# Optimization experiments

Hardware: AMD Instinct MI355X
Metric: run time of the kernel (lower is better)

The kernel has to match this reference:

```python
import jax, jax.numpy as jnp
import numpy as np

NEG = -1e9  # mask value for non-edges (matches masked_fill(-inf) numerically-safely)
SLOPE = 0.2  # LeakyReLU negative slope in GraphAttentionLayer


def gat_layer(x, W, a_l, a_r, adj, n_heads):
    """One GraphAttentionLayer (eval mode, is_concat=True).
    e[i,j,h] = leakyrelu(a_l . g[i,h] + a_r . g[j,h])  (attn Linear split into halves)
    softmax over j masked by adj, then aggregate neighbors.
    """
    n = x.shape[0]
    g = (x @ W).reshape(n, n_heads, -1)          # [n, h, f]
    el = jnp.einsum('ihf,f->ih', g, a_l)          # score contribution of node i
    er = jnp.einsum('jhf,f->jh', g, a_r)          # score contribution of node j
    e = jax.nn.leaky_relu(el[:, None, :] + er[None, :, :], SLOPE)  # [n, n, h]
    e = jnp.where(adj[:, :, None] != 0, e, NEG)
    a = jax.nn.softmax(e, axis=1)                 # softmax over neighbors j
    out = jnp.einsum('ijh,jhf->ihf', a, g)        # weighted aggregation
    return out.reshape(n, -1)                     # concat heads


def setup_inputs() -> dict:
    key = jax.random.key(0)
    ks = jax.random.split(key, 8)
    N, IN, HID, OUT, H = 2048, 512, 256, 128, 8
    x = jax.random.normal(ks[0], (N, IN), dtype=jnp.float32)
    adj = jax.random.randint(ks[1], (N, N), 0, 2, dtype=jnp.int32)
    adj = adj.at[jnp.arange(N), jnp.arange(N)].set(1)  # self loops: no empty softmax rows
    s = 0.05
    W1 = jax.random.normal(ks[2], (IN, HID), dtype=jnp.float32) * s
    a1_l = jax.random.normal(ks[3], (HID // H,), dtype=jnp.float32) * s
    a1_r = jax.random.normal(ks[4], (HID // H,), dtype=jnp.float32) * s
    W2 = jax.random.normal(ks[5], (HID, OUT), dtype=jnp.float32) * s
    a2_l = jax.random.normal(ks[6], (OUT,), dtype=jnp.float32) * s
    a2_r = jax.random.normal(ks[7], (OUT,), dtype=jnp.float32) * s
    return {"x": x, "W1": W1, "a1_l": a1_l, "a1_r": a1_r,
            "W2": W2, "a2_l": a2_l, "a2_r": a2_r, "adj_mat": adj}


def reference(x, W1, a1_l, a1_r, W2, a2_l, a2_r, adj_mat):
    # eval mode: nn.Dropout is identity
    h = gat_layer(x, W1, a1_l, a1_r, adj_mat, n_heads=8)
    h = jax.nn.elu(h)
    out = gat_layer(h, W2, a2_l, a2_r, adj_mat, n_heads=1)
    return out
```

## Files before the change

kernel.cpp:

```cpp
#include <hip/hip_runtime.h>
#include <hip/hip_bf16.h>

#define NN 2048
typedef unsigned short u16;
typedef unsigned long long u64;
typedef __attribute__((ext_vector_type(8))) short short8;
typedef __attribute__((ext_vector_type(4))) float f32x4;

__device__ __forceinline__ unsigned bfb(float x) {
    unsigned u = __float_as_uint(x);
    return (u + 0x7FFFu + ((u >> 16) & 1u)) >> 16;
}
__device__ __forceinline__ unsigned pk2(float a, float b) {
    unsigned r;
    asm("v_cvt_pk_bf16_f32 %0, %1, %2" : "=v"(r) : "v"(a), "v"(b));
    return r;
}

__global__ __launch_bounds__(256) void prep(const float* __restrict__ x,
                                            const float* __restrict__ W1,
                                            const float* __restrict__ W2,
                                            const int* __restrict__ adj,
                                            u16* __restrict__ xb, u16* __restrict__ w1t,
                                            u16* __restrict__ w2t, u64* __restrict__ ab) {
    const int b = blockIdx.x;
    const int tid = threadIdx.x;
    if (b < 2048) {
#pragma unroll
        for (int k = 0; k < 8; ++k) {
            int t = (b * 8 + k) * 256 + tid;
            int W = t >> 6, lane = t & 63;
            int i = W >> 5, jw = W & 31;
            int a = adj[(size_t)i * NN + jw * 64 + lane];
            u64 mk = __ballot(a != 0);
            if (lane == 0) ab[(size_t)i * 32 + jw] = mk;
        }
    } else if (b < 2048 + 256) {
#pragma unroll
        for (int k = 0; k < 4; ++k) {
            int t = ((b - 2048) * 4 + k) * 256 + tid;
            float4 v = ((const float4*)x)[t];
            uint2 o;
            o.x = pk2(v.x, v.y);
            o.y = pk2(v.z, v.w);
            ((uint2*)xb)[t] = o;
        }
    } else if (b < 2048 + 256 + 128) {
#pragma unroll
        for (int k = 0; k < 4; ++k) {
            int u = ((b - 2304) * 4 + k) * 256 + tid;
            int c = u >> 9, kk = u & 511;
            w1t[u] = (u16)bfb(W1[(size_t)kk * 256 + c]);
        }
    } else {
#pragma unroll
        for (int k = 0; k < 4; ++k) {
            int u = ((b - 2432) * 4 + k) * 256 + tid;
            int c = u >> 8, kk = u & 255;
            w2t[u] = (u16)bfb(W2[(size_t)kk * 128 + c]);
        }
    }
}

__global__ __launch_bounds__(256) void gemm1(const u16* __restrict__ A,
                                             const u16* __restrict__ BT,
                                             const float* __restrict__ al,
                                             const float* __restrict__ ar,
                                             u16* __restrict__ GT,
                                             float* __restrict__ el,
                                             float* __restrict__ ert) {
    const int i0 = blockIdx.x * 16, cs = blockIdx.y;
    const int t = threadIdx.x, lane = t & 63, w = t >> 6;
    const int q = lane >> 4, n = lane & 15;
    const int ct = w & 1, kh = w >> 1;
    __shared__ float osh[2][16][16];
    __shared__ float pel[2][16], per_[2][16];

    const u16* ap = A + (size_t)(i0 + n) * 512 + kh * 256 + q * 8;
    const u16* bp = BT + (size_t)(cs * 32 + ct * 16 + n) * 512 + kh * 256 + q * 8;
    f32x4 acc = {0.f, 0.f, 0.f, 0.f};
#pragma unroll
    for (int ks = 0; ks < 8; ++ks) {
        short8 a = *(const short8*)(ap + ks * 32);
        short8 b = *(const short8*)(bp + ks * 32);
        acc = __builtin_amdgcn_mfma_f32_16x16x32_bf16(a, b, acc, 0, 0, 0);
    }
    if (kh == 1) {
#pragma unroll
        for (int r = 0; r < 4; ++r) osh[ct][q * 4 + r][n] = acc[r];
    }
    __syncthreads();
    if (kh == 0) {
#pragma unroll
        for (int r = 0; r < 4; ++r) acc[r] += osh[ct][q * 4 + r][n];
        uint2 g0;
        g0.x = pk2(acc[0], acc[1]);
        g0.y = pk2(acc[2], acc[3]);
        *(uint2*)&GT[(size_t)(cs * 32 + ct * 16 + n) * NN + i0 + q * 4] = g0;
        const float alv = al[ct * 16 + n], arv = ar[ct * 16 + n];
#pragma unroll
        for (int r = 0; r < 4; ++r) {
            float ve = acc[r] * alv, vr = acc[r] * arv;
#pragma unroll
            for (int off = 1; off <= 8; off <<= 1) {
                ve += __shfl_xor(ve, off);
                vr += __shfl_xor(vr, off);
            }
            if (n == 0) { pel[ct][q * 4 + r] = ve; per_[ct][q * 4 + r] = vr; }
        }
    }
    __syncthreads();
    if (t < 16) {
        el[(size_t)(i0 + t) * 8 + cs] = pel[0][t] + pel[1][t];
        ert[(size_t)cs * NN + i0 + t] = per_[0][t] + per_[1][t];
    }
}

__global__ __launch_bounds__(256) void gemm2(const u16* __restrict__ A,
                                             const u16* __restrict__ BT,
                                             const float* __restrict__ al,
                                             const float* __restrict__ ar,
                                             u16* __restrict__ GT,
                                             float* __restrict__ el2p,
                                             float* __restrict__ er2p) {
    const int i0 = blockIdx.x * 16, cs = blockIdx.y;
    const int t = threadIdx.x, lane = t & 63, w = t >> 6;
    const int q = lane >> 4, n = lane & 15;
    const int ct = w & 1, kh = w >> 1;
    __shared__ float osh[2][16][16];
    __shared__ float pel[2][16], per_[2][16];

    const u16* ap = A + (size_t)(i0 + n) * 256 + kh * 128 + q * 8;
    const u16* bp = BT + (size_t)(cs * 32 + ct * 16 + n) * 256 + kh * 128 + q * 8;
    f32x4 acc = {0.f, 0.f, 0.f, 0.f};
#pragma unroll
    for (int ks = 0; ks < 4; ++ks) {
        short8 a = *(const short8*)(ap + ks * 32);
        short8 b = *(const short8*)(bp + ks * 32);
        acc = __builtin_amdgcn_mfma_f32_16x16x32_bf16(a, b, acc, 0, 0, 0);
    }
    if (kh == 1) {
#pragma unroll
        for (int r = 0; r < 4; ++r) osh[ct][q * 4 + r][n] = acc[r];
    }
    __syncthreads();
    if (kh == 0) {
#pragma unroll
        for (int r = 0; r < 4; ++r) acc[r] += osh[ct][q * 4 + r][n];
        uint2 g0;
        g0.x = pk2(acc[0], acc[1]);
        g0.y = pk2(acc[2], acc[3]);
        *(uint2*)&GT[(size_t)(cs * 32 + ct * 16 + n) * NN + i0 + q * 4] = g0;
        const float alv = al[cs * 32 + ct * 16 + n], arv = ar[cs * 32 + ct * 16 + n];
#pragma unroll
        for (int r = 0; r < 4; ++r) {
            float ve = acc[r] * alv, vr = acc[r] * arv;
#pragma unroll
            for (int off = 1; off <= 8; off <<= 1) {
                ve += __shfl_xor(ve, off);
                vr += __shfl_xor(vr, off);
            }
            if (n == 0) { pel[ct][q * 4 + r] = ve; per_[ct][q * 4 + r] = vr; }
        }
    }
    __syncthreads();
    if (t < 16) {
        el2p[(size_t)cs * NN + i0 + t] = pel[0][t] + pel[1][t];
        er2p[(size_t)cs * NN + i0 + t] = per_[0][t] + per_[1][t];
    }
}

__global__ __launch_bounds__(512, 4) void attn1(const float* __restrict__ el,
                                                const float* __restrict__ ert,
                                                const unsigned* __restrict__ ab32,
                                                const u16* __restrict__ gbt,
                                                u16* __restrict__ hbb) {
    const int rt = blockIdx.x, sec = blockIdx.y;
    const int i0 = rt * 16, h0 = sec * 2;
    const int t = threadIdx.x, lane = t & 63, w = t >> 6;
    const int q = lane >> 4, n = lane & 15;
    const int m = t >> 5, jq = t & 31;
    const int hl = w >> 2, ch = (w >> 1) & 1, kf2 = w & 1;

    __shared__ u16 ersb[2][2048];
    __shared__ __align__(16) u16 pl[2][2][16][264];
    __shared__ unsigned absh[16][64];
    __shared__ float psum_sh[16][2];
    __shared__ float osh[2][2][16][16];
    __shared__ float wmax[2][8];
    __shared__ float mxsh[2];

    float4 v0 = *(const float4*)(ert + (size_t)h0 * NN + t * 4);
    float4 v1 = *(const float4*)(ert + (size_t)(h0 + 1) * NN + t * 4);
    uint2 c0, c1;
    c0.x = pk2(v0.x, v0.y); c0.y = pk2(v0.z, v0.w);
    c1.x = pk2(v1.x, v1.y); c1.y = pk2(v1.z, v1.w);
    *(uint2*)&ersb[0][t * 4] = c0;
    *(uint2*)&ersb[1][t * 4] = c1;
    float m0 = fmaxf(fmaxf(v0.x, v0.y), fmaxf(v0.z, v0.w));
    float m1 = fmaxf(fmaxf(v1.x, v1.y), fmaxf(v1.z, v1.w));
#pragma unroll
    for (int off = 32; off; off >>= 1) {
        m0 = fmaxf(m0, __shfl_xor(m0, off));
        m1 = fmaxf(m1, __shfl_xor(m1, off));
    }
    if (lane == 0) { wmax[0][w] = m0; wmax[1][w] = m1; }
    for (int c = t; c < 1024; c += 512)
        absh[c >> 6][c & 63] = ab32[(size_t)(i0 + (c >> 6)) * 64 + (c & 63)];
    __syncthreads();
    if (t < 2) {
        float mm = wmax[t][0];
#pragma unroll
        for (int ww = 1; ww < 8; ++ww) mm = fmaxf(mm, wmax[t][ww]);
        mxsh[t] = mm;
    }
    __syncthreads();

    float elv[2], mxv[2], ps[2];
#pragma unroll
    for (int h = 0; h < 2; ++h) {
        float e = el[(size_t)(i0 + m) * 8 + h0 + h];
        elv[h] = e;
        float mm = e + mxsh[h];
        mxv[h] = fmaxf(mm, 0.2f * mm);
        ps[h] = 0.f;
    }

    auto stage = [&](int tl, int nb) {
#pragma unroll
        for (int sub = 0; sub < 2; ++sub) {
            unsigned word = absh[m][tl * 8 + sub * 4 + (jq >> 3)];
            unsigned bits = (word >> ((jq & 7) * 4)) & 0xFu;
            const int jo = tl * 256 + sub * 128 + jq * 4;
            uint2 raw0 = *(const uint2*)&ersb[0][jo];
            uint2 raw1 = *(const uint2*)&ersb[1][jo];
#pragma unroll
            for (int h = 0; h < 2; ++h) {
                uint2 raw = h ? raw1 : raw0;
                float e0 = __uint_as_float(raw.x << 16);
                float e1 = __uint_as_float(raw.x & 0xFFFF0000u);
                float e2 = __uint_as_float(raw.y << 16);
                float e3 = __uint_as_float(raw.y & 0xFFFF0000u);
                float s0 = elv[h] + e0, s1 = elv[h] + e1, s2 = elv[h] + e2, s3 = elv[h] + e3;
                s0 = fmaxf(s0, 0.2f * s0) - mxv[h];
                s1 = fmaxf(s1, 0.2f * s1) - mxv[h];
                s2 = fmaxf(s2, 0.2f * s2) - mxv[h];
                s3 = fmaxf(s3, 0.2f * s3) - mxv[h];
                float p0 = (bits & 1u) ? __expf(s0) : 0.f;
                float p1 = (bits & 2u) ? __expf(s1) : 0.f;
                float p2 = (bits & 4u) ? __expf(s2) : 0.f;
                float p3 = (bits & 8u) ? __expf(s3) : 0.f;
                ps[h] += (p0 + p1) + (p2 + p3);
                uint2 pkv;
                pkv.x = pk2(p0, p1);
                pkv.y = pk2(p2, p3);
                *(uint2*)&pl[nb][h][m][sub * 128 + jq * 4] = pkv;
            }
        }
    };

    const int col = sec * 64 + hl * 32 + ch * 16 + n;
    const u16* gb = gbt + (size_t)col * NN + kf2 * 128 + q * 8;
    short8 bc0 = *(const short8*)gb;
    short8 bc1 = *(const short8*)(gb + 32);
    short8 bc2 = *(const short8*)(gb + 64);
    short8 bc3 = *(const short8*)(gb + 96);
    f32x4 acc = {0.f, 0.f, 0.f, 0.f};

    stage(0, 0);
    __syncthreads();

    for (int tile = 0; tile < 8; ++tile) {
        short8 bn0 = bc0, bn1 = bc1, bn2 = bc2, bn3 = bc3;
        if (tile < 7) {
            const u16* gq = gb + (tile + 1) * 256;
            bn0 = *(const short8*)gq;
            bn1 = *(const short8*)(gq + 32);
            bn2 = *(const short8*)(gq + 64);
            bn3 = *(const short8*)(gq + 96);
        }
        const u16* ap = &pl[tile & 1][hl][n][kf2 * 128 + q * 8];
        short8 a0 = *(const short8*)ap;
        short8 a1 = *(const short8*)(ap + 32);
        short8 a2 = *(const short8*)(ap + 64);
        short8 a3 = *(const short8*)(ap + 96);
        acc = __builtin_amdgcn_mfma_f32_16x16x32_bf16(a0, bc0, acc, 0, 0, 0);
        acc = __builtin_amdgcn_mfma_f32_16x16x32_bf16(a1, bc1, acc, 0, 0, 0);
        acc = __builtin_amdgcn_mfma_f32_16x16x32_bf16(a2, bc2, acc, 0, 0, 0);
        acc = __builtin_amdgcn_mfma_f32_16x16x32_bf16(a3, bc3, acc, 0, 0, 0);
        if (tile < 7) stage(tile + 1, (tile + 1) & 1);
        bc0 = bn0; bc1 = bn1; bc2 = bn2; bc3 = bn3;
        __syncthreads();
    }

#pragma unroll
    for (int h = 0; h < 2; ++h) {
        float v = ps[h];
#pragma unroll
        for (int off = 16; off; off >>= 1) v += __shfl_down(v, off, 32);
        if (jq == 0) psum_sh[m][h] = v;
    }
    if (kf2 == 1) {
#pragma unroll
        for (int r = 0; r < 4; ++r) osh[hl][ch][q * 4 + r][n] = acc[r];
    }
    __syncthreads();
    if (kf2 == 0) {
#pragma unroll
        for (int r = 0; r < 4; ++r) {
            int mr = q * 4 + r;
            float o = (acc[r] + osh[hl][ch][mr][n]) / psum_sh[mr][hl];
            o = o > 0.f ? o : (__expf(o) - 1.f);
            hbb[(size_t)(i0 + mr) * 256 + col] = (u16)bfb(o);
        }
    }
}

__global__ __launch_bounds__(512) void attn2(const float* __restrict__ el2p,
                                             const float* __restrict__ er2p,
                                             const unsigned* __restrict__ ab32,
                                             const u16* __restrict__ gbt,
                                             float* __restrict__ out) {
    const int rt = blockIdx.x, sec = blockIdx.y;
    const int i0 = rt * 16;
    const int t = threadIdx.x, lane = t & 63, w = t >> 6;
    const int q = lane >> 4, n = lane & 15;
    const int m = t >> 5, jq = t & 31;
    const int ct = w >> 1, kf2 = w & 1;

    __shared__ u16 ersb[2048];
    __shared__ __align__(16) u16 pl[2][16][264];
    __shared__ unsigned absh[16][64];
    __shared__ float psum_sh[16];
    __shared__ float osh[4][16][16];
    __shared__ float wmax[8];
    __shared__ float mxsh;

    float4 a0 = *(const float4*)(er2p + t * 4);
    float4 a1 = *(const float4*)(er2p + NN + t * 4);
    float4 a2 = *(const float4*)(er2p + 2 * NN + t * 4);
    float4 a3 = *(const float4*)(er2p + 3 * NN + t * 4);
    float4 v0;
    v0.x = ((a0.x + a1.x) + (a2.x + a3.x));
    v0.y = ((a0.y + a1.y) + (a2.y + a3.y));
    v0.z = ((a0.z + a1.z) + (a2.z + a3.z));
    v0.w = ((a0.w + a1.w) + (a2.w + a3.w));
    uint2 c0;
    c0.x = pk2(v0.x, v0.y); c0.y = pk2(v0.z, v0.w);
    *(uint2*)&ersb[t * 4] = c0;
    float m0 = fmaxf(fmaxf(v0.x, v0.y), fmaxf(v0.z, v0.w));
#pragma unroll
    for (int off = 32; off; off >>= 1) m0 = fmaxf(m0, __shfl_xor(m0, off));
    if (lane == 0) wmax[w] = m0;
    for (int c = t; c < 1024; c += 512)
        absh[c >> 6][c & 63] = ab32[(size_t)(i0 + (c >> 6)) * 64 + (c & 63)];
    __syncthreads();
    if (t == 0) {
        float mm = wmax[0];
#pragma unroll
        for (int ww = 1; ww < 8; ++ww) mm = fmaxf(mm, wmax[ww]);
        mxsh = mm;
    }
    __syncthreads();

    const float elv = el2p[i0 + m] + el2p[NN + i0 + m] + el2p[2 * NN + i0 + m] + el2p[3 * NN + i0 + m];
    float mm2 = elv + mxsh;
    const float mxv = fmaxf(mm2, 0.2f * mm2);
    float ps = 0.f;

    auto stage = [&](int tl, int nb) {
#pragma unroll
        for (int sub = 0; sub < 2; ++sub) {
            unsigned word = absh[m][tl * 8 + sub * 4 + (jq >> 3)];
            unsigned bits = (word >> ((jq & 7) * 4)) & 0xFu;
            const int jo = tl * 256 + sub * 128 + jq * 4;
            uint2 raw = *(const uint2*)&ersb[jo];
            float e0 = __uint_as_float(raw.x << 16);
            float e1 = __uint_as_float(raw.x & 0xFFFF0000u);
            float e2 = __uint_as_float(raw.y << 16);
            float e3 = __uint_as_float(raw.y & 0xFFFF0000u);
            float s0 = elv + e0, s1 = elv + e1, s2 = elv + e2, s3 = elv + e3;
            s0 = fmaxf(s0, 0.2f * s0) - mxv;
            s1 = fmaxf(s1, 0.2f * s1) - mxv;
            s2 = fmaxf(s2, 0.2f * s2) - mxv;
            s3 = fmaxf(s3, 0.2f * s3) - mxv;
            float p0 = (bits & 1u) ? __expf(s0) : 0.f;
            float p1 = (bits & 2u) ? __expf(s1) : 0.f;
            float p2 = (bits & 4u) ? __expf(s2) : 0.f;
            float p3 = (bits & 8u) ? __expf(s3) : 0.f;
            ps += (p0 + p1) + (p2 + p3);
            uint2 pkv;
            pkv.x = pk2(p0, p1);
            pkv.y = pk2(p2, p3);
            *(uint2*)&pl[nb][m][sub * 128 + jq * 4] = pkv;
        }
    };

    const int col = sec * 64 + ct * 16 + n;
    const u16* gb = gbt + (size_t)col * NN + kf2 * 128 + q * 8;
    short8 bc0 = *(const short8*)gb;
    short8 bc1 = *(const short8*)(gb + 32);
    short8 bc2 = *(const short8*)(gb + 64);
    short8 bc3 = *(const short8*)(gb + 96);
    f32x4 acc = {0.f, 0.f, 0.f, 0.f};

    stage(0, 0);
    __syncthreads();

    for (int tile = 0; tile < 8; ++tile) {
        short8 bn0 = bc0, bn1 = bc1, bn2 = bc2, bn3 = bc3;
        if (tile < 7) {
            const u16* gq = gb + (tile + 1) * 256;
            bn0 = *(const short8*)gq;
            bn1 = *(const short8*)(gq + 32);
            bn2 = *(const short8*)(gq + 64);
            bn3 = *(const short8*)(gq + 96);
        }
        const u16* ap = &pl[tile & 1][n][kf2 * 128 + q * 8];
        short8 a0v = *(const short8*)ap;
        short8 a1v = *(const short8*)(ap + 32);
        short8 a2v = *(const short8*)(ap + 64);
        short8 a3v = *(const short8*)(ap + 96);
        acc = __builtin_amdgcn_mfma_f32_16x16x32_bf16(a0v, bc0, acc, 0, 0, 0);
        acc = __builtin_amdgcn_mfma_f32_16x16x32_bf16(a1v, bc1, acc, 0, 0, 0);
        acc = __builtin_amdgcn_mfma_f32_16x16x32_bf16(a2v, bc2, acc, 0, 0, 0);
        acc = __builtin_amdgcn_mfma_f32_16x16x32_bf16(a3v, bc3, acc, 0, 0, 0);
        if (tile < 7) stage(tile + 1, (tile + 1) & 1);
        bc0 = bn0; bc1 = bn1; bc2 = bn2; bc3 = bn3;
        __syncthreads();
    }

#pragma unroll
    for (int off = 16; off; off >>= 1) ps += __shfl_down(ps, off, 32);
    if (jq == 0) psum_sh[m] = ps;
    if (kf2 == 1) {
#pragma unroll
        for (int r = 0; r < 4; ++r) osh[ct][q * 4 + r][n] = acc[r];
    }
    __syncthreads();
    if (kf2 == 0) {
#pragma unroll
        for (int r = 0; r < 4; ++r) {
            int mr = q * 4 + r;
            out[(size_t)(i0 + mr) * 128 + col] = (acc[r] + osh[ct][mr][n]) / psum_sh[mr];
        }
    }
}

extern "C" void kernel_launch(void* const* d_in, const int* in_sizes, int n_in,
                              void* d_out, int out_size, void* d_ws, size_t ws_size,
                              hipStream_t stream) {
    const float* x   = (const float*)d_in[0];
    const float* W1  = (const float*)d_in[1];
    const float* a1l = (const float*)d_in[2];
    const float* a1r = (const float*)d_in[3];
    const float* W2  = (const float*)d_in[4];
    const float* a2l = (const float*)d_in[5];
    const float* a2r = (const float*)d_in[6];
    const int* adj = (const int*)d_in[7];

    char* p = (char*)d_ws;
    u16* xb    = (u16*)p;            p += (size_t)NN * 512 * 2;
    u16* w1t   = (u16*)p;            p += (size_t)256 * 512 * 2;
    u16* w2t   = (u16*)p;            p += (size_t)128 * 256 * 2;
    unsigned* abits = (unsigned*)p;  p += (size_t)NN * 64 * 4;
    u16* gbt1  = (u16*)p;            p += (size_t)256 * NN * 2;
    u16* hbb   = (u16*)p;            p += (size_t)NN * 256 * 2;
    u16* gbt2  = (u16*)p;            p += (size_t)128 * NN * 2;
    float* el1 = (float*)p;          p += (size_t)NN * 8 * 4;
    float* ert1 = (float*)p;         p += (size_t)8 * NN * 4;
    float* el2p = (float*)p;         p += (size_t)4 * NN * 4;
    float* er2p = (float*)p;         p += (size_t)4 * NN * 4;

    prep<<<2464, 256, 0, stream>>>(x, W1, W2, adj, xb, w1t, w2t, (u64*)abits);

    gemm1<<<dim3(128, 8), 256, 0, stream>>>(xb, w1t, a1l, a1r, gbt1, el1, ert1);
    attn1<<<dim3(128, 4), 512, 0, stream>>>(el1, ert1, abits, gbt1, hbb);

    gemm2<<<dim3(128, 4), 256, 0, stream>>>(hbb, w2t, a2l, a2r, gbt2, el2p, er2p);
    attn2<<<dim3(128, 2), 512, 0, stream>>>(el2p, er2p, abits, gbt2, (float*)d_out);
}
```

Measured before the change: 126.2 us.

## Fuse prep conversion into GEMM kernels and fold adjacency bitpacking into gemm1

Removes the separate prep kernel. Each GEMM block now loads fp32 x and W tiles directly, converts them to bf16 into padded LDS, and runs MFMA from shared memory. Adjacency bit-packing runs in extra gemm1 grid blocks (cs>=8). This saves a launch and the bf16 staging round trip through global memory. In exchange, every block redundantly converts its W slice and reads W with strided, uncoalesced accesses, and the adj packing now runs on only 256 blocks.

After: 139.2 us. +10.3%, slower.

```diff
diff --git a/kernel.cpp b/kernel.cpp
--- a/kernel.cpp
+++ b/kernel.cpp
@@ -17,74 +17,74 @@
     return r;
 }
 
-__global__ __launch_bounds__(256) void prep(const float* __restrict__ x,
-                                            const float* __restrict__ W1,
-                                            const float* __restrict__ W2,
-                                            const int* __restrict__ adj,
-                                            u16* __restrict__ xb, u16* __restrict__ w1t,
-                                            u16* __restrict__ w2t, u64* __restrict__ ab) {
-    const int b = blockIdx.x;
-    const int tid = threadIdx.x;
-    if (b < 2048) {
-#pragma unroll
-        for (int k = 0; k < 8; ++k) {
-            int t = (b * 8 + k) * 256 + tid;
-            int W = t >> 6, lane = t & 63;
-            int i = W >> 5, jw = W & 31;
-            int a = adj[(size_t)i * NN + jw * 64 + lane];
-            u64 mk = __ballot(a != 0);
-            if (lane == 0) ab[(size_t)i * 32 + jw] = mk;
-        }
-    } else if (b < 2048 + 256) {
-#pragma unroll
-        for (int k = 0; k < 4; ++k) {
-            int t = ((b - 2048) * 4 + k) * 256 + tid;
-            float4 v = ((const float4*)x)[t];
-            uint2 o;
-            o.x = pk2(v.x, v.y);
-            o.y = pk2(v.z, v.w);
-            ((uint2*)xb)[t] = o;
-        }
-    } else if (b < 2048 + 256 + 128) {
-#pragma unroll
-        for (int k = 0; k < 4; ++k) {
-            int u = ((b - 2304) * 4 + k) * 256 + tid;
-            int c = u >> 9, kk = u & 511;
-            w1t[u] = (u16)bfb(W1[(size_t)kk * 256 + c]);
-        }
-    } else {
-#pragma unroll
-        for (int k = 0; k < 4; ++k) {
-            int u = ((b - 2432) * 4 + k) * 256 + tid;
-            int c = u >> 8, kk = u & 255;
-            w2t[u] = (u16)bfb(W2[(size_t)kk * 128 + c]);
-        }
-    }
-}
-
-__global__ __launch_bounds__(256) void gemm1(const u16* __restrict__ A,
-                                             const u16* __restrict__ BT,
+__global__ __launch_bounds__(256) void gemm1(const float* __restrict__ x,
+                                             const float* __restrict__ W1,
+                                             const int* __restrict__ adj,
                                              const float* __restrict__ al,
                                              const float* __restrict__ ar,
                                              u16* __restrict__ GT,
                                              float* __restrict__ el,
-                                             float* __restrict__ ert) {
-    const int i0 = blockIdx.x * 16, cs = blockIdx.y;
-    const int t = threadIdx.x, lane = t & 63, w = t >> 6;
+                                             float* __restrict__ ert,
+                                             u64* __restrict__ ab) {
+    const int rt = blockIdx.x, cs = blockIdx.y;
+    const int t = threadIdx.x;
+    if (cs >= 8) {
+        const int b = (cs - 8) * 128 + rt;
+        const int r0 = b * 8;
+        const int lane = t & 63;
+#pragma unroll 4
+        for (int k = 0; k < 64; ++k) {
+            int tl = k * 256 + t;
+            int W = tl >> 6;
+            int rl = W >> 5, jw = W & 31;
+            int a = adj[(size_t)(r0 + rl) * NN + jw * 64 + lane];
+            u64 mk = __ballot(a != 0);
+            if (lane == 0) ab[(size_t)(r0 + rl) * 32 + jw] = mk;
+        }
+        return;
+    }
+    const int i0 = rt * 16;
+    const int lane = t & 63, w = t >> 6;
     const int q = lane >> 4, n = lane & 15;
     const int ct = w & 1, kh = w >> 1;
+    __shared__ __align__(16) u16 As[16][520];
+    __shared__ __align__(16) u16 Bs[32][520];
     __shared__ float osh[2][16][16];
     __shared__ float pel[2][16], per_[2][16];
 
-    const u16* ap = A + (size_t)(i0 + n) * 512 + kh * 256 + q * 8;
-    const u16* bp = BT + (size_t)(cs * 32 + ct * 16 + n) * 512 + kh * 256 + q * 8;
+    {
+        const float4* xs = (const float4*)(x + (size_t)i0 * 512);
+#pragma unroll
+        for (int j = 0; j < 8; ++j) {
+            float4 v = xs[j * 256 + t];
+            int off = (j * 256 + t) * 4;
+            int r = off >> 9, k = off & 511;
+            uint2 o;
+            o.x = pk2(v.x, v.y);
+            o.y = pk2(v.z, v.w);
+            *(uint2*)&As[r][k] = o;
+        }
+    }
+    {
+        const int cl = t & 31, kr0 = t >> 5;
+#pragma unroll 4
+        for (int it = 0; it < 64; ++it) {
+            int k = it * 8 + kr0;
+            Bs[cl][k] = (u16)bfb(W1[(size_t)k * 256 + cs * 32 + cl]);
+        }
+    }
+    __syncthreads();
+
+    const u16* apl = &As[n][kh * 256 + q * 8];
+    const u16* bpl = &Bs[ct * 16 + n][kh * 256 + q * 8];
     f32x4 acc = {0.f, 0.f, 0.f, 0.f};
 #pragma unroll
     for (int ks = 0; ks < 8; ++ks) {
-        short8 a = *(const short8*)(ap + ks * 32);
-        short8 b = *(const short8*)(bp + ks * 32);
+        short8 a = *(const short8*)(apl + ks * 32);
+        short8 b = *(const short8*)(bpl + ks * 32);
         acc = __builtin_amdgcn_mfma_f32_16x16x32_bf16(a, b, acc, 0, 0, 0);
     }
+    __syncthreads();
     if (kh == 1) {
 #pragma unroll
         for (int r = 0; r < 4; ++r) osh[ct][q * 4 + r][n] = acc[r];
@@ -117,7 +117,7 @@
 }
 
 __global__ __launch_bounds__(256) void gemm2(const u16* __restrict__ A,
-                                             const u16* __restrict__ BT,
+                                             const float* __restrict__ W2,
                                              const float* __restrict__ al,
                                              const float* __restrict__ ar,
                                              u16* __restrict__ GT,
@@ -127,18 +127,41 @@
     const int t = threadIdx.x, lane = t & 63, w = t >> 6;
     const int q = lane >> 4, n = lane & 15;
     const int ct = w & 1, kh = w >> 1;
+    __shared__ __align__(16) u16 As[16][264];
+    __shared__ __align__(16) u16 Bs[32][264];
     __shared__ float osh[2][16][16];
     __shared__ float pel[2][16], per_[2][16];
 
-    const u16* ap = A + (size_t)(i0 + n) * 256 + kh * 128 + q * 8;
-    const u16* bp = BT + (size_t)(cs * 32 + ct * 16 + n) * 256 + kh * 128 + q * 8;
+    {
+        const uint2* hs = (const uint2*)(A + (size_t)i0 * 256);
+#pragma unroll
+        for (int j = 0; j < 4; ++j) {
+            uint2 v = hs[j * 256 + t];
+            int off = (j * 256 + t) * 4;
+            int r = off >> 8, k = off & 255;
+            *(uint2*)&As[r][k] = v;
+        }
+    }
+    {
+        const int cl = t & 31, kr0 = t >> 5;
+#pragma unroll 4
+        for (int it = 0; it < 32; ++it) {
+            int k = it * 8 + kr0;
+            Bs[cl][k] = (u16)bfb(W2[(size_t)k * 128 + cs * 32 + cl]);
+        }
+    }
+    __syncthreads();
+
+    const u16* apl = &As[n][kh * 128 + q * 8];
+    const u16* bpl = &Bs[ct * 16 + n][kh * 128 + q * 8];
     f32x4 acc = {0.f, 0.f, 0.f, 0.f};
 #pragma unroll
     for (int ks = 0; ks < 4; ++ks) {
-        short8 a = *(const short8*)(ap + ks * 32);
-        short8 b = *(const short8*)(bp + ks * 32);
+        short8 a = *(const short8*)(apl + ks * 32);
+        short8 b = *(const short8*)(bpl + ks * 32);
         acc = __builtin_amdgcn_mfma_f32_16x16x32_bf16(a, b, acc, 0, 0, 0);
     }
+    __syncthreads();
     if (kh == 1) {
 #pragma unroll
         for (int r = 0; r < 4; ++r) osh[ct][q * 4 + r][n] = acc[r];
@@ -460,9 +483,6 @@
     const int* adj = (const int*)d_in[7];
 
     char* p = (char*)d_ws;
-    u16* xb    = (u16*)p;            p += (size_t)NN * 512 * 2;
-    u16* w1t   = (u16*)p;            p += (size_t)256 * 512 * 2;
-    u16* w2t   = (u16*)p;            p += (size_t)128 * 256 * 2;
     unsigned* abits = (unsigned*)p;  p += (size_t)NN * 64 * 4;
     u16* gbt1  = (u16*)p;            p += (size_t)256 * NN * 2;
     u16* hbb   = (u16*)p;            p += (size_t)NN * 256 * 2;
@@ -472,11 +492,9 @@
     float* el2p = (float*)p;         p += (size_t)4 * NN * 4;
     float* er2p = (float*)p;         p += (size_t)4 * NN * 4;
 
-    prep<<<2464, 256, 0, stream>>>(x, W1, W2, adj, xb, w1t, w2t, (u64*)abits);
-
-    gemm1<<<dim3(128, 8), 256, 0, stream>>>(xb, w1t, a1l, a1r, gbt1, el1, ert1);
+    gemm1<<<dim3(128, 10), 256, 0, stream>>>(x, W1, adj, a1l, a1r, gbt1, el1, ert1, (u64*)abits);
     attn1<<<dim3(128, 4), 512, 0, stream>>>(el1, ert1, abits, gbt1, hbb);
 
-    gemm2<<<dim3(128, 4), 256, 0, stream>>>(hbb, w2t, a2l, a2r, gbt2, el2p, er2p);
+    gemm2<<<dim3(128, 4), 256, 0, stream>>>(hbb, W2, a2l, a2r, gbt2, el2p, er2p);
     attn2<<<dim3(128, 2), 512, 0, stream>>>(el2p, er2p, abits, gbt2, (float*)d_out);
 }
```

## Stage GEMM operand tiles through swizzled LDS and remap gemm1 blocks per XCD

Applied to the files above, without the earlier changes.

Both projection GEMMs now copy their A and B tiles cooperatively into shared memory with coalesced 8-byte loads and an XOR swizzle, then feed the MFMAs from LDS instead of issuing strided per-lane global loads. gemm1 also moves to a 1D grid whose block index is remapped so that row tiles sharing the same XCD are grouped together, which aims to improve L2 locality. This adds LDS footprint and a barrier before compute, while the global traffic per block stays the same.

After: 124.6 us. No clear change (-1.2%).

```diff
diff --git a/kernel.cpp b/kernel.cpp
--- a/kernel.cpp
+++ b/kernel.cpp
@@ -62,28 +62,55 @@
     }
 }
 
-__global__ __launch_bounds__(256) void gemm1(const u16* __restrict__ A,
-                                             const u16* __restrict__ BT,
+__global__ __launch_bounds__(256) void gemm1(const u16* __restrict__ xb,
+                                             const u16* __restrict__ w1t,
                                              const float* __restrict__ al,
                                              const float* __restrict__ ar,
                                              u16* __restrict__ GT,
                                              float* __restrict__ el,
                                              float* __restrict__ ert) {
-    const int i0 = blockIdx.x * 16, cs = blockIdx.y;
+    const int bid = blockIdx.x;
+    const int xcd = bid & 7, idx = bid >> 3;
+    const int rt = xcd * 16 + (idx & 15), cs = idx >> 4;
+    const int i0 = rt * 16;
     const int t = threadIdx.x, lane = t & 63, w = t >> 6;
     const int q = lane >> 4, n = lane & 15;
     const int ct = w & 1, kh = w >> 1;
+    __shared__ __align__(16) u16 As[16][520];
+    __shared__ __align__(16) u16 Bs[32][520];
     __shared__ float osh[2][16][16];
     __shared__ float pel[2][16], per_[2][16];
 
-    const u16* ap = A + (size_t)(i0 + n) * 512 + kh * 256 + q * 8;
-    const u16* bp = BT + (size_t)(cs * 32 + ct * 16 + n) * 512 + kh * 256 + q * 8;
+    {
+        const uint2* xs = (const uint2*)(xb + (size_t)i0 * 512);
+#pragma unroll
+        for (int j = 0; j < 8; ++j) {
+            uint2 v = xs[j * 256 + t];
+            int e = (j * 256 + t) * 4;
+            int r = e >> 9, k = e & 511;
+            *(uint2*)&As[r][k ^ ((r & 7) << 3)] = v;
+        }
+    }
+    {
+        const uint2* bsrc = (const uint2*)(w1t + (size_t)cs * 32 * 512);
+#pragma unroll
+        for (int j = 0; j < 16; ++j) {
+            uint2 v = bsrc[j * 256 + t];
+            int e = (j * 256 + t) * 4;
+            int r = e >> 9, k = e & 511;
+            *(uint2*)&Bs[r][k ^ ((r & 7) << 3)] = v;
+        }
+    }
+    __syncthreads();
+
+    const int an = n, bn = ct * 16 + n;
+    const int k0 = kh * 256 + q * 8;
     f32x4 acc = {0.f, 0.f, 0.f, 0.f};
 #pragma unroll
     for (int ks = 0; ks < 8; ++ks) {
-        short8 a = *(const short8*)(ap + ks * 32);
-        short8 b = *(const short8*)(bp + ks * 32);
-        acc = __builtin_amdgcn_mfma_f32_16x16x32_bf16(a, b, acc, 0, 0, 0);
+        short8 a = *(const short8*)&As[an][(k0 + ks * 32) ^ ((an & 7) << 3)];
+        short8 bb = *(const short8*)&Bs[bn][(k0 + ks * 32) ^ ((bn & 7) << 3)];
+        acc = __builtin_amdgcn_mfma_f32_16x16x32_bf16(a, bb, acc, 0, 0, 0);
     }
     if (kh == 1) {
 #pragma unroll
@@ -117,7 +144,7 @@
 }
 
 __global__ __launch_bounds__(256) void gemm2(const u16* __restrict__ A,
-                                             const u16* __restrict__ BT,
+                                             const u16* __restrict__ w2t,
                                              const float* __restrict__ al,
                                              const float* __restrict__ ar,
                                              u16* __restrict__ GT,
@@ -127,17 +154,41 @@
     const int t = threadIdx.x, lane = t & 63, w = t >> 6;
     const int q = lane >> 4, n = lane & 15;
     const int ct = w & 1, kh = w >> 1;
+    __shared__ __align__(16) u16 As[16][264];
+    __shared__ __align__(16) u16 Bs[32][264];
     __shared__ float osh[2][16][16];
     __shared__ float pel[2][16], per_[2][16];
 
-    const u16* ap = A + (size_t)(i0 + n) * 256 + kh * 128 + q * 8;
-    const u16* bp = BT + (size_t)(cs * 32 + ct * 16 + n) * 256 + kh * 128 + q * 8;
+    {
+        const uint2* hs = (const uint2*)(A + (size_t)i0 * 256);
+#pragma unroll
+        for (int j = 0; j < 4; ++j) {
+            uint2 v = hs[j * 256 + t];
+            int e = (j * 256 + t) * 4;
+            int r = e >> 8, k = e & 255;
+            *(uint2*)&As[r][k ^ ((r & 7) << 3)] = v;
+        }
+    }
+    {
+        const uint2* bsrc = (const uint2*)(w2t + (size_t)cs * 32 * 256);
+#pragma unroll
+        for (int j = 0; j < 8; ++j) {
+            uint2 v = bsrc[j * 256 + t];
+            int e = (j * 256 + t) * 4;
+            int r = e >> 8, k = e & 255;
+            *(uint2*)&Bs[r][k ^ ((r & 7) << 3)] = v;
+        }
+    }
+    __syncthreads();
+
+    const int an = n, bn = ct * 16 + n;
+    const int k0 = kh * 128 + q * 8;
     f32x4 acc = {0.f, 0.f, 0.f, 0.f};
 #pragma unroll
     for (int ks = 0; ks < 4; ++ks) {
-        short8 a = *(const short8*)(ap + ks * 32);
-        short8 b = *(const short8*)(bp + ks * 32);
-        acc = __builtin_amdgcn_mfma_f32_16x16x32_bf16(a, b, acc, 0, 0, 0);
+        short8 a = *(const short8*)&As[an][(k0 + ks * 32) ^ ((an & 7) << 3)];
+        short8 bb = *(const short8*)&Bs[bn][(k0 + ks * 32) ^ ((bn & 7) << 3)];
+        acc = __builtin_amdgcn_mfma_f32_16x16x32_bf16(a, bb, acc, 0, 0, 0);
     }
     if (kh == 1) {
 #pragma unroll
@@ -474,7 +525,7 @@
 
     prep<<<2464, 256, 0, stream>>>(x, W1, W2, adj, xb, w1t, w2t, (u64*)abits);
 
-    gemm1<<<dim3(128, 8), 256, 0, stream>>>(xb, w1t, a1l, a1r, gbt1, el1, ert1);
+    gemm1<<<1024, 256, 0, stream>>>(xb, w1t, a1l, a1r, gbt1, el1, ert1);
     attn1<<<dim3(128, 4), 512, 0, stream>>>(el1, ert1, abits, gbt1, hbb);
 
     gemm2<<<dim3(128, 4), 256, 0, stream>>>(hbb, w2t, a2l, a2r, gbt2, el2p, er2p);
```
